# Kernel tuning notes

Measured on AMD Instinct MI355X. Metric: run time of the kernel, lower is better.

## Reference

```python
import jax, jax.numpy as jnp
import numpy as np

B, S, HID = 1, 2048, 2048
H = 16
D_NOPE, D_ROPE, D_V = 128, 64, 128
Q_HEAD = D_NOPE + D_ROPE  # 192
QL, KVL = 1536, 512
EPS = 1e-6
SCALE = Q_HEAD ** -0.5


def rms_norm(x, w, eps=EPS):
    return x * jax.lax.rsqrt(jnp.mean(x * x, axis=-1, keepdims=True) + eps) * w


def rotate_half(x):
    h = x.shape[-1] // 2
    return jnp.concatenate([-x[..., h:], x[..., :h]], axis=-1)


def apply_rope(x, cos, sin):
    # DeepSeek de-interleave: view(..., d//2, 2).transpose(-1,-2).reshape == [even, odd]
    x = jnp.concatenate([x[..., 0::2], x[..., 1::2]], axis=-1)
    return x * cos + rotate_half(x) * sin


def setup_inputs() -> dict:
    key = jax.random.key(0)
    ks = jax.random.split(key, 8)
    x = jax.random.normal(ks[0], (B, S, HID), dtype=jnp.float32)
    # causal additive mask
    causal = jnp.tril(jnp.ones((S, S), dtype=bool))
    mask = jnp.where(causal, 0.0, -1e9).astype(jnp.float32)[None, None]
    position_ids = jnp.broadcast_to(jnp.arange(S, dtype=jnp.int32), (B, S))
    # RoPE caches, theta=10000
    inv_freq = 1.0 / (10000.0 ** (np.arange(0, D_ROPE, 2, dtype=np.float32) / D_ROPE))
    freqs = np.outer(np.arange(S, dtype=np.float32), inv_freq)
    emb = np.concatenate([freqs, freqs], axis=-1)
    cos = jnp.asarray(np.cos(emb), dtype=jnp.float32)
    sin = jnp.asarray(np.sin(emb), dtype=jnp.float32)
    w = lambda k, shp: (jax.random.normal(k, shp, dtype=jnp.float32) * 0.02)
    return {
        "x": x, "mask": mask, "position_ids": position_ids, "cos": cos, "sin": sin,
        "q_a_w": w(ks[1], (HID, QL)),
        "q_a_ln": jnp.ones((QL,), jnp.float32),
        "q_b_w": w(ks[2], (QL, H * Q_HEAD)),
        "kv_a_w": w(ks[3], (HID, KVL + D_ROPE)),
        "kv_a_ln": jnp.ones((KVL,), jnp.float32),
        "kv_b_w": w(ks[4], (KVL, H * (D_NOPE + D_V))),
        "o_w": w(ks[5], (H * D_V, HID)),
    }


def reference(x, mask, position_ids, cos, sin, q_a_w, q_a_ln, q_b_w, kv_a_w, kv_a_ln, kv_b_w, o_w):
    b, s, _ = x.shape
    # low-rank Q projection
    q = rms_norm(x @ q_a_w, q_a_ln) @ q_b_w            # [B,S,H*192]
    q = q.reshape(b, s, H, Q_HEAD).transpose(0, 2, 1, 3)  # [B,H,S,192]
    q_nope, q_pe = q[..., :D_NOPE], q[..., D_NOPE:]
    # compressed KV + decoupled rope key (MQA, shared across heads)
    ckv = x @ kv_a_w                                   # [B,S,512+64]
    c_norm = rms_norm(ckv[..., :KVL], kv_a_ln)         # [B,S,512]
    k_pe = ckv[..., KVL:][:, None]                     # [B,1,S,64]
    kv = (c_norm @ kv_b_w).reshape(b, s, H, D_NOPE + D_V).transpose(0, 2, 1, 3)
    k_nope, value = kv[..., :D_NOPE], kv[..., D_NOPE:]  # [B,H,S,128] each
    # rope
    cos_p = cos[position_ids][:, None]                 # [B,1,S,64]
    sin_p = sin[position_ids][:, None]
    q_pe = apply_rope(q_pe, cos_p, sin_p)
    k_pe = apply_rope(k_pe, cos_p, sin_p)
    query = jnp.concatenate([q_nope, q_pe], axis=-1)   # [B,H,S,192]
    key = jnp.concatenate([k_nope, jnp.broadcast_to(k_pe, (b, H, s, D_ROPE))], axis=-1)
    scores = jnp.einsum("bhsd,bhtd->bhst", query, key) * SCALE + mask
    attn = jax.nn.softmax(scores, axis=-1)
    out = jnp.einsum("bhst,bhtd->bhsd", attn, value)   # [B,H,S,128]
    out = out.transpose(0, 2, 1, 3).reshape(b, s, H * D_V) @ o_w
    kv_cache = jnp.concatenate([c_norm, k_pe[:, 0]], axis=-1)  # [B,S,576] latent cache
    return out, kv_cache
```

## Files before the change

### kernel.cpp

```cpp
#include <hip/hip_runtime.h>

typedef unsigned short u16;
typedef __bf16 bf16x8 __attribute__((ext_vector_type(8)));
typedef short s16x4 __attribute__((ext_vector_type(4)));
typedef short s16x8 __attribute__((ext_vector_type(8)));
typedef float f32x4 __attribute__((ext_vector_type(4)));

#define S_LEN 2048
#define NHEAD 16
#define QHEAD 192
#define EPS 1e-6f
#define ATTN_SCALE 0.07216878364870323f
#define QSCALE_LOG2E 0.10412011228586118f

__device__ __forceinline__ u16 f2bf(float f) {
    unsigned u = __builtin_bit_cast(unsigned, f);
    u = (u + 0x7FFFu + ((u >> 16) & 1u)) >> 16;
    return (u16)u;
}
__device__ __forceinline__ float bf2f(u16 h) {
    unsigned u = ((unsigned)h) << 16;
    return __builtin_bit_cast(float, u);
}

__device__ __forceinline__ void gl_lds16(const u16* g, u16* l) {
    __builtin_amdgcn_global_load_lds(
        (const __attribute__((address_space(1))) unsigned int*)g,
        (__attribute__((address_space(3))) unsigned int*)l,
        16, 0, 0);
}

#if defined(__has_builtin) && __has_builtin(__builtin_amdgcn_mfma_f32_16x16x16bf16_1k)
__device__ __forceinline__ f32x4 mfma16(s16x4 a, s16x4 b, f32x4 c) {
    return __builtin_amdgcn_mfma_f32_16x16x16bf16_1k(a, b, c, 0, 0, 0);
}
#else
__device__ __forceinline__ f32x4 mfma16(s16x4 a, s16x4 b, f32x4 c) {
    asm volatile("v_mfma_f32_16x16x16_bf16 %0, %1, %2, %0"
                 : "+v"(c) : "v"(a), "v"(b));
    return c;
}
#endif

template <int CF32>
__device__ __forceinline__ void gemm_core(
    u16* __restrict__ smem,
    const u16* __restrict__ A, const u16* __restrict__ B, void* __restrict__ Cv,
    int K, int lda, int ldb, int ldc, int tm, int tn)
{
    const int tid = threadIdx.x;
    const int w = tid >> 6, lane = tid & 63;
    const int q = lane >> 4, r = lane & 15;

    const int lr = lane & 15;
    const int lc = (lane >> 4) * 8;
    const u16* ga0 = A + (long)(tm * 128 + w * 32 + lr) * lda + lc;
    const u16* ga1 = ga0 + 16 * (long)lda;
    const u16* gb0 = B + (long)(tn * 128 + w * 32 + lr) * ldb + lc;
    const u16* gb1 = gb0 + 16 * (long)ldb;
    const int sa0 = w * 1024, sa1 = sa0 + 512;
    const int sb0 = 4096 + w * 1024, sb1 = sb0 + 512;

    f32x4 acc[4][4] = {};
    const int wm = w >> 1;
    const int wn = w & 1;
    const int n = K >> 6;

    gl_lds16(ga0, smem + sa0);
    gl_lds16(ga1, smem + sa1);
    gl_lds16(gb0, smem + sb0);
    gl_lds16(gb1, smem + sb1);
    gl_lds16(ga0 + 32, smem + 8192 + sa0);
    gl_lds16(ga1 + 32, smem + 8192 + sa1);
    gl_lds16(gb0 + 32, smem + 8192 + sb0);
    gl_lds16(gb1 + 32, smem + 8192 + sb1);
    asm volatile("s_waitcnt vmcnt(0)" ::: "memory");
    __builtin_amdgcn_sched_barrier(0);
    __builtin_amdgcn_s_barrier();
    __builtin_amdgcn_sched_barrier(0);

    for (int t = 0; t < n; ++t) {
        u16* const cur = smem + (t & 1) * 16384;
        u16* const nxt = smem + ((t + 1) & 1) * 16384;
        if (t + 1 < n) {
            const long k1 = (long)(t + 1) << 6;
            gl_lds16(ga0 + k1, nxt + sa0);
            gl_lds16(ga1 + k1, nxt + sa1);
            gl_lds16(gb0 + k1, nxt + sb0);
            gl_lds16(gb1 + k1, nxt + sb1);
            gl_lds16(ga0 + k1 + 32, nxt + 8192 + sa0);
            gl_lds16(ga1 + k1 + 32, nxt + 8192 + sa1);
            gl_lds16(gb0 + k1 + 32, nxt + 8192 + sb0);
            gl_lds16(gb1 + k1 + 32, nxt + 8192 + sb1);
        }
        #pragma unroll
        for (int kk = 0; kk < 2; ++kk) {
            u16* const sub = cur + kk * 8192;
            bf16x8 af[4], bv[4];
            #pragma unroll
            for (int mt = 0; mt < 4; ++mt)
                af[mt] = *(const bf16x8*)&sub[(wm * 4 + mt) * 512 + lane * 8];
            #pragma unroll
            for (int nt = 0; nt < 4; ++nt)
                bv[nt] = *(const bf16x8*)&sub[4096 + (wn * 4 + nt) * 512 + lane * 8];
            #pragma unroll
            for (int mt = 0; mt < 4; ++mt)
                #pragma unroll
                for (int nt = 0; nt < 4; ++nt)
                    acc[mt][nt] = __builtin_amdgcn_mfma_f32_16x16x32_bf16(
                        af[mt], bv[nt], acc[mt][nt], 0, 0, 0);
        }
        if (t + 1 < n) {
            asm volatile("s_waitcnt vmcnt(0)" ::: "memory");
            __builtin_amdgcn_sched_barrier(0);
            __builtin_amdgcn_s_barrier();
            __builtin_amdgcn_sched_barrier(0);
        }
    }

    const int row0 = tm * 128 + wm * 64 + q * 4;
    const int col0 = tn * 128 + wn * 64 + r;
    if (CF32) {
        float* C = (float*)Cv;
        #pragma unroll
        for (int mt = 0; mt < 4; ++mt)
            #pragma unroll
            for (int i = 0; i < 4; ++i) {
                long rb = (long)(row0 + mt * 16 + i) * ldc + col0;
                #pragma unroll
                for (int nt = 0; nt < 4; ++nt)
                    C[rb + nt * 16] = acc[mt][nt][i];
            }
    } else {
        u16* C = (u16*)Cv;
        #pragma unroll
        for (int mt = 0; mt < 4; ++mt)
            #pragma unroll
            for (int i = 0; i < 4; ++i) {
                long rb = (long)(row0 + mt * 16 + i) * ldc + col0;
                #pragma unroll
                for (int nt = 0; nt < 4; ++nt)
                    C[rb + nt * 16] = f2bf(acc[mt][nt][i]);
            }
    }
}

__global__ __launch_bounds__(256, 2)
void gemm_ks(const u16* __restrict__ A, const u16* __restrict__ B,
             float* __restrict__ C0, float* __restrict__ C1,
             int Kh, int lda, int ldb, int ldc)
{
    __shared__ __align__(16) u16 smem[2 * 16384];
    const int z = blockIdx.z;
    float* C = z ? C1 : C0;
    gemm_core<1>(smem, A + (long)z * Kh, B + (long)z * Kh, C,
                 Kh, lda, ldb, ldc, blockIdx.y, blockIdx.x);
}

__global__ __launch_bounds__(256, 2)
void gemm_bt_dual(const u16* __restrict__ A0, const u16* __restrict__ B0,
                  void* __restrict__ C0, int K0, int lda0, int ldb0, int ldc0, int nx0,
                  const u16* __restrict__ A1, const u16* __restrict__ B1,
                  void* __restrict__ C1, int K1, int lda1, int ldb1, int ldc1, int nx1)
{
    __shared__ __align__(16) u16 smem[2 * 16384];
    if (blockIdx.z == 0) {
        if ((int)blockIdx.x >= nx0) return;
        gemm_core<0>(smem, A0, B0, C0, K0, lda0, ldb0, ldc0,
                     blockIdx.y, blockIdx.x);
    } else {
        if ((int)blockIdx.x >= nx1) return;
        gemm_core<0>(smem, A1, B1, C1, K1, lda1, ldb1, ldc1,
                     blockIdx.y, blockIdx.x);
    }
}

__global__ __launch_bounds__(256)
void addout_k(float4* __restrict__ out, const float4* __restrict__ p)
{
    int i = blockIdx.x * 256 + threadIdx.x;
    float4 a = out[i], b = p[i];
    a.x += b.x; a.y += b.y; a.z += b.z; a.w += b.w;
    out[i] = a;
}

template<int C0, int C1>
__device__ __forceinline__ void stage_tile(
    const u16* __restrict__ kvb, const u16* __restrict__ kpe,
    const u16* __restrict__ vt,
    u16* __restrict__ Kl, u16* __restrict__ Vl,
    int h, int t, int quad, int r)
{
    #pragma unroll
    for (int c = C0; c < C1; ++c) {
        if (c < 24) {
            const int mtk = c / 6, kc = c % 6;
            const int row = t * 64 + mtk * 16 + r;
            const u16* src = (kc < 4)
                ? kvb + (size_t)row * 4096 + h * 256 + kc * 32 + quad * 8
                : kpe + (size_t)row * 64 + (kc - 4) * 32 + quad * 8;
            gl_lds16(src, &Kl[c * 512]);
        } else {
            const int cv = c - 24, mtd = cv >> 1, sc = cv & 1;
            const u16* src = vt + ((size_t)h * 128 + mtd * 16 + r) * 2048
                             + t * 64 + sc * 32 + quad * 8;
            gl_lds16(src, &Vl[cv * 512]);
        }
    }
}

__device__ __forceinline__ void stage_dispatch(
    const u16* __restrict__ kvb, const u16* __restrict__ kpe,
    const u16* __restrict__ vt,
    u16* __restrict__ Kl, u16* __restrict__ Vl,
    int w, int h, int t, int quad, int r)
{
    if (w == 0)      stage_tile<0, 10>(kvb, kpe, vt, Kl, Vl, h, t, quad, r);
    else if (w == 1) stage_tile<10, 20>(kvb, kpe, vt, Kl, Vl, h, t, quad, r);
    else if (w == 2) stage_tile<20, 30>(kvb, kpe, vt, Kl, Vl, h, t, quad, r);
    else             stage_tile<30, 40>(kvb, kpe, vt, Kl, Vl, h, t, quad, r);
}

__device__ __forceinline__ void kv_tile_step(
    const u16* __restrict__ Kl, const u16* __restrict__ Vl,
    const bf16x8 (&Qf)[6], f32x4 (&Oacc)[8], float& lsum,
    int lane, int quad, int r, int kglob0, int qg, bool maskT)
{
    f32x4 Sacc[4];
    #pragma unroll
    for (int mtk = 0; mtk < 4; ++mtk)
        Sacc[mtk] = (f32x4){0.f, 0.f, 0.f, 0.f};
    #pragma unroll
    for (int kc = 0; kc < 6; ++kc)
        #pragma unroll
        for (int mtk = 0; mtk < 4; ++mtk) {
            bf16x8 Ak = *(const bf16x8*)&Kl[(mtk * 6 + kc) * 512 + lane * 8];
            Sacc[mtk] = __builtin_amdgcn_mfma_f32_16x16x32_bf16(
                Ak, Qf[kc], Sacc[mtk], 0, 0, 0);
        }
    #pragma unroll
    for (int sc = 0; sc < 2; ++sc) {
        s16x4 Pf[2];
        #pragma unroll
        for (int half = 0; half < 2; ++half) {
            const int kb = sc * 2 + half;
            const int kb0 = kglob0 + kb * 16 + quad * 4;
            #pragma unroll
            for (int i = 0; i < 4; ++i) {
                float pv = exp2f(Sacc[kb][i]);
                if (maskT && (kb0 + i > qg)) pv = 0.f;
                lsum += pv;
                Pf[half][i] = (short)f2bf(pv);
            }
        }
        #pragma unroll
        for (int mtd = 0; mtd < 8; ++mtd) {
            s16x8 Av8 = *(const s16x8*)&Vl[(mtd * 2 + sc) * 512 + quad * 128 + r * 8];
            s16x4 lo = __builtin_shufflevector(Av8, Av8, 0, 1, 2, 3);
            s16x4 hi = __builtin_shufflevector(Av8, Av8, 4, 5, 6, 7);
            Oacc[mtd] = mfma16(lo, Pf[0], Oacc[mtd]);
            Oacc[mtd] = mfma16(hi, Pf[1], Oacc[mtd]);
        }
    }
}

__global__ __launch_bounds__(256, 2)
void flash_attn(const u16* __restrict__ query, const u16* __restrict__ kvb,
                const u16* __restrict__ kpe, const u16* __restrict__ vt,
                u16* __restrict__ ao)
{
    const int tid = threadIdx.x;
    const int w = tid >> 6, lane = tid & 63;
    const int quad = lane >> 4, r = lane & 15;

    const int bid = (int)blockIdx.x;
    const int i = bid & 255;
    const int t_ = i >> 4;
    const int h = i & 15;
    const int j = (bid < 256) ? (31 - t_) : t_;

    const int q0 = j * 64;
    const int ntk = j + 1;

    __shared__ __align__(16) u16 smem[40960];

    const int qg = q0 + w * 16 + r;

    bf16x8 Qf[6];
    #pragma unroll
    for (int kc = 0; kc < 6; ++kc)
        Qf[kc] = *(const bf16x8*)(query
            + ((size_t)h * S_LEN + q0 + w * 16 + r) * QHEAD
            + kc * 32 + quad * 8);

    f32x4 Oacc[8];
    #pragma unroll
    for (int mtd = 0; mtd < 8; ++mtd)
        Oacc[mtd] = (f32x4){0.f, 0.f, 0.f, 0.f};
    float lsum = 0.f;

    stage_dispatch(kvb, kpe, vt, smem, smem + 12288, w, h, 0, quad, r);
    __syncthreads();

    for (int t = 0; t < ntk; ++t) {
        u16* const curb = smem + (t & 1) * 20480;
        u16* const nxtb = smem + ((t + 1) & 1) * 20480;
        if (t + 1 < ntk)
            stage_dispatch(kvb, kpe, vt, nxtb, nxtb + 12288, w, h, t + 1, quad, r);
        kv_tile_step(curb, curb + 12288, Qf, Oacc, lsum,
                     lane, quad, r, t * 64, qg, t == ntk - 1);
        __syncthreads();
    }

    float l = lsum;
    l += __shfl_xor(l, 16, 64);
    l += __shfl_xor(l, 32, 64);
    const float inv = 1.0f / l;
    const int qrow = q0 + w * 16 + r;
    #pragma unroll
    for (int mtd = 0; mtd < 8; ++mtd) {
        ushort4 o;
        o.x = f2bf(Oacc[mtd][0] * inv);
        o.y = f2bf(Oacc[mtd][1] * inv);
        o.z = f2bf(Oacc[mtd][2] * inv);
        o.w = f2bf(Oacc[mtd][3] * inv);
        *(ushort4*)(ao + (size_t)qrow * 2048 + h * 128 + mtd * 16 + quad * 4) = o;
    }
}

__device__ __forceinline__ void wtrans_body(
    float (*tile)[33], const float* __restrict__ in, u16* __restrict__ out,
    int K, int N, int bx, int by, int tid)
{
    const int tx = tid & 31, ty = tid >> 5;
    const int k0 = bx * 32, n0 = by * 32;
    #pragma unroll
    for (int jj = 0; jj < 32; jj += 8) {
        int nn = n0 + tx;
        tile[ty + jj][tx] = (nn < N) ? in[(long)(k0 + ty + jj) * N + nn] : 0.0f;
    }
    __syncthreads();
    #pragma unroll
    for (int jj = 0; jj < 32; jj += 8)
        out[(long)(n0 + ty + jj) * K + k0 + tx] = f2bf(tile[tx][ty + jj]);
}

__global__ __launch_bounds__(256)
void prep_k(const float4* __restrict__ x4, ushort4* __restrict__ xb4,
            const float* __restrict__ q_a_w, const float* __restrict__ kv_a_w,
            const float* __restrict__ q_b_w, const float* __restrict__ kv_b_w,
            const float* __restrict__ o_w,
            u16* __restrict__ W1, u16* __restrict__ qbwt,
            u16* __restrict__ kvbwt, u16* __restrict__ owt)
{
    __shared__ float tile[32][33];
    const int tid = threadIdx.x;
    int b = (int)blockIdx.x;
    if (b < 4096) {
        int i = b * 256 + tid;
        float4 v = x4[i];
        ushort4 o;
        o.x = f2bf(v.x); o.y = f2bf(v.y); o.z = f2bf(v.z); o.w = f2bf(v.w);
        xb4[i] = o;
        return;
    }
    b -= 4096;
    if (b < 3072)       wtrans_body(tile, q_a_w,  W1,                  2048, 1536, b % 64, b / 64, tid);
    else if ((b -= 3072) < 1280) wtrans_body(tile, kv_a_w, W1 + 1536ULL * 2048, 2048, 576,  b % 64, b / 64, tid);
    else if ((b -= 1280) < 4608) wtrans_body(tile, q_b_w,  qbwt,       1536, 3072, b % 48, b / 48, tid);
    else if ((b -= 4608) < 2048) wtrans_body(tile, kv_b_w, kvbwt,      512,  4096, b % 16, b / 16, tid);
    else { b -= 2048;            wtrans_body(tile, o_w,    owt,        2048, 2048, b % 64, b / 64, tid); }
}

__global__ __launch_bounds__(256)
void norm_k(const float* __restrict__ pa, const float* __restrict__ pb,
            u16* __restrict__ qkv, const float* __restrict__ q_ln,
            const float* __restrict__ kv_ln, const int* __restrict__ pos_ids,
            const float* __restrict__ cosb, const float* __restrict__ sinb,
            float* __restrict__ kvout, u16* __restrict__ cnb,
            u16* __restrict__ kpe)
{
    const int s = blockIdx.x, tid = threadIdx.x;
    __shared__ float rowbuf[2176];
    __shared__ float red[8];
    const long base = (long)s * 2176;
    float sum1 = 0.f, sum2 = 0.f;
    for (int d = tid; d < 2176; d += 256) {
        float v = pa[base + d] + pb[base + d];
        rowbuf[d] = v;
        if (d < 1536)      sum1 += v * v;
        else if (d < 2048) sum2 += v * v;
    }
    #pragma unroll
    for (int o = 32; o; o >>= 1) {
        sum1 += __shfl_xor(sum1, o, 64);
        sum2 += __shfl_xor(sum2, o, 64);
    }
    if ((tid & 63) == 0) { red[tid >> 6] = sum1; red[4 + (tid >> 6)] = sum2; }
    __syncthreads();
    sum1 = red[0] + red[1] + red[2] + red[3];
    sum2 = red[4] + red[5] + red[6] + red[7];
    const float sc1 = rsqrtf(sum1 / 1536.f + EPS);
    const float sc2 = rsqrtf(sum2 / 512.f + EPS);
    for (int d = tid; d < 1536; d += 256)
        qkv[base + d] = f2bf(rowbuf[d] * sc1 * q_ln[d]);
    for (int d = tid; d < 512; d += 256) {
        float v = rowbuf[1536 + d] * sc2 * kv_ln[d];
        kvout[(long)s * 576 + d] = v;
        cnb[(long)s * 512 + d] = f2bf(v);
    }
    if (tid < 32) {
        int p = pos_ids[s];
        float x0 = rowbuf[2048 + 2 * tid];
        float x1 = rowbuf[2048 + 2 * tid + 1];
        float c1 = cosb[p * 64 + tid], s1 = sinb[p * 64 + tid];
        float c2 = cosb[p * 64 + 32 + tid], s2 = sinb[p * 64 + 32 + tid];
        float lo = x0 * c1 - x1 * s1;
        float hi = x1 * c2 + x0 * s2;
        kvout[(long)s * 576 + 512 + tid] = lo;
        kvout[(long)s * 576 + 544 + tid] = hi;
        kpe[(long)s * 64 + tid] = f2bf(lo);
        kpe[(long)s * 64 + 32 + tid] = f2bf(hi);
    }
}

__global__ __launch_bounds__(256)
void post_k(const u16* __restrict__ qb, const int* __restrict__ pos_ids,
            const float* __restrict__ cosb, const float* __restrict__ sinb,
            u16* __restrict__ query, const u16* __restrict__ kv,
            u16* __restrict__ vt)
{
    __shared__ u16 tile[32][33];
    const int tid = threadIdx.x;
    int b = (int)blockIdx.x;
    if (b < 2048) {
        const int s = b;
        const u16* row = qb + (long)s * 3072;
        {
            int h = tid >> 4, c = tid & 15;
            const u16* src = &row[h * QHEAD + c * 8];
            u16* dst = &query[((long)(h * S_LEN + s)) * QHEAD + c * 8];
            ushort4 a = *(const ushort4*)src;
            ushort4 bb = *(const ushort4*)(src + 4);
            ushort4 oa, ob;
            oa.x = f2bf(bf2f(a.x) * QSCALE_LOG2E); oa.y = f2bf(bf2f(a.y) * QSCALE_LOG2E);
            oa.z = f2bf(bf2f(a.z) * QSCALE_LOG2E); oa.w = f2bf(bf2f(a.w) * QSCALE_LOG2E);
            ob.x = f2bf(bf2f(bb.x) * QSCALE_LOG2E); ob.y = f2bf(bf2f(bb.y) * QSCALE_LOG2E);
            ob.z = f2bf(bf2f(bb.z) * QSCALE_LOG2E); ob.w = f2bf(bf2f(bb.w) * QSCALE_LOG2E);
            *(ushort4*)dst = oa;
            *(ushort4*)(dst + 4) = ob;
        }
        int p = pos_ids[s];
        for (int idx = tid; idx < 512; idx += 256) {
            int h = idx >> 5, i = idx & 31;
            float x0 = bf2f(row[h * QHEAD + 128 + 2 * i]);
            float x1 = bf2f(row[h * QHEAD + 128 + 2 * i + 1]);
            float c1 = cosb[p * 64 + i], s1 = sinb[p * 64 + i];
            float c2 = cosb[p * 64 + 32 + i], s2 = sinb[p * 64 + 32 + i];
            u16* qr = query + ((long)(h * S_LEN + s)) * QHEAD;
            qr[128 + i] = f2bf((x0 * c1 - x1 * s1) * QSCALE_LOG2E);
            qr[160 + i] = f2bf((x1 * c2 + x0 * s2) * QSCALE_LOG2E);
        }
    } else {
        b -= 2048;
        const int s0 = (b & 63) * 32, d0 = ((b >> 6) & 3) * 32, h = b >> 8;
        const int tx = tid & 31, ty = tid >> 5;
        #pragma unroll
        for (int jj = 0; jj < 32; jj += 8)
            tile[ty + jj][tx] = kv[(long)(s0 + ty + jj) * 4096 + h * 256 + 128 + d0 + tx];
        __syncthreads();
        const int txp = ((tx >> 2) & 3) * 8 + (tx >> 4) * 4 + (tx & 3);
        #pragma unroll
        for (int jj = 0; jj < 32; jj += 8)
            vt[(long)(h * 128 + d0 + ty + jj) * S_LEN + s0 + txp] = tile[tx][ty + jj];
    }
}

extern "C" void kernel_launch(void* const* d_in, const int* in_sizes, int n_in,
                              void* d_out, int out_size, void* d_ws, size_t ws_size,
                              hipStream_t stream)
{
    const float* x      = (const float*)d_in[0];
    const int*   posid  = (const int*)d_in[2];
    const float* cosb   = (const float*)d_in[3];
    const float* sinb   = (const float*)d_in[4];
    const float* q_a_w  = (const float*)d_in[5];
    const float* q_a_ln = (const float*)d_in[6];
    const float* q_b_w  = (const float*)d_in[7];
    const float* kv_a_w = (const float*)d_in[8];
    const float* kv_a_ln= (const float*)d_in[9];
    const float* kv_b_w = (const float*)d_in[10];
    const float* o_w    = (const float*)d_in[11];

    float* out    = (float*)d_out;
    float* kv_out = out + (size_t)2048 * 2048;

    char* ws = (char*)d_ws;
    size_t off = 0;
    auto alloc = [&](size_t bytes) { char* p = ws + off; off += (bytes + 255) & ~(size_t)255; return p; };
    u16* xb    = (u16*)alloc(2048ULL * 2048 * 2);
    u16* W1    = (u16*)alloc(2176ULL * 2048 * 2);
    u16* qbwt  = (u16*)alloc(3072ULL * 1536 * 2);
    u16* kvbwt = (u16*)alloc(4096ULL * 512 * 2);
    u16* owt   = (u16*)alloc(2048ULL * 2048 * 2);
    u16* qkv_a = (u16*)alloc(2048ULL * 2176 * 2);
    u16* qbuf  = (u16*)alloc(2048ULL * 3072 * 2);
    u16* query = (u16*)alloc(16ULL * 2048 * 192 * 2);
    u16* cnb   = (u16*)alloc(2048ULL * 512 * 2);
    u16* kpe   = (u16*)alloc(2048ULL * 64 * 2);
    u16* kvbuf = (u16*)alloc(2048ULL * 4096 * 2);
    u16* vt    = (u16*)alloc(16ULL * 128 * 2048 * 2);
    u16* ao    = (u16*)alloc(2048ULL * 2048 * 2);
    (void)ws_size; (void)in_sizes; (void)n_in; (void)out_size;

    float* g1p0 = (float*)qbuf;
    float* g1p1 = (float*)kvbuf;
    float* g5p  = (float*)xb;

    dim3 blk(256);

    prep_k<<<dim3(19200), blk, 0, stream>>>(
        (const float4*)x, (ushort4*)xb, q_a_w, kv_a_w, q_b_w, kv_b_w, o_w,
        W1, qbwt, kvbwt, owt);

    gemm_ks<<<dim3(17, 16, 2), blk, 0, stream>>>(
        xb, W1, g1p0, g1p1, 1024, 2048, 2048, 2176);

    norm_k<<<dim3(2048), blk, 0, stream>>>(g1p0, g1p1, qkv_a, q_a_ln, kv_a_ln,
                                           posid, cosb, sinb, kv_out, cnb, kpe);

    gemm_bt_dual<<<dim3(32, 16, 2), blk, 0, stream>>>(
        qkv_a, qbwt, qbuf, 1536, 2176, 1536, 3072, 24,
        cnb, kvbwt, kvbuf, 512, 512, 512, 4096, 32);

    post_k<<<dim3(6144), blk, 0, stream>>>(qbuf, posid, cosb, sinb, query, kvbuf, vt);

    flash_attn<<<dim3(512), dim3(256), 0, stream>>>(query, kvbuf, kpe, vt, ao);

    gemm_ks<<<dim3(16, 16, 2), blk, 0, stream>>>(
        ao, owt, g5p, out, 1024, 2048, 2048, 2048);
    addout_k<<<dim3(4096), blk, 0, stream>>>((float4*)out, (const float4*)g5p);
}
```

Measured before the change: 390.6 us.

## Split attention KV range across two blocks, merge partials, overlap weight transposes with GEMM

Flash attention now splits each query tile's KV loop into two halves handled by separate blocks (1024 blocks instead of 512). Each block writes unnormalized fp32 partial outputs and row sums, and a new merge kernel combines them into bf16. The q_b, kv_b and o weight transposes move out of the prep kernel and into the first GEMM's launch as extra blocks, so that work overlaps with the GEMM. s_setprio is raised around the attention compute step. The split adds fp32 partial traffic and an extra launch, and depends on workspace aliasing (PA on xb, PB on qbwt, lp on cnb) being safe at that point in the pipeline.

```diff
diff --git a/kernel.cpp b/kernel.cpp
--- a/kernel.cpp
+++ b/kernel.cpp
@@ -145,6 +145,23 @@
     }
 }
 
+__device__ __forceinline__ void wtrans_body(
+    float (*tile)[33], const float* __restrict__ in, u16* __restrict__ out,
+    int K, int N, int bx, int by, int tid)
+{
+    const int tx = tid & 31, ty = tid >> 5;
+    const int k0 = bx * 32, n0 = by * 32;
+    #pragma unroll
+    for (int jj = 0; jj < 32; jj += 8) {
+        int nn = n0 + tx;
+        tile[ty + jj][tx] = (nn < N) ? in[(long)(k0 + ty + jj) * N + nn] : 0.0f;
+    }
+    __syncthreads();
+    #pragma unroll
+    for (int jj = 0; jj < 32; jj += 8)
+        out[(long)(n0 + ty + jj) * K + k0 + tx] = f2bf(tile[tx][ty + jj]);
+}
+
 __global__ __launch_bounds__(256, 2)
 void gemm_ks(const u16* __restrict__ A, const u16* __restrict__ B,
              float* __restrict__ C0, float* __restrict__ C1,
@@ -155,6 +172,30 @@
     float* C = z ? C1 : C0;
     gemm_core<1>(smem, A + (long)z * Kh, B + (long)z * Kh, C,
                  Kh, lda, ldb, ldc, blockIdx.y, blockIdx.x);
+}
+
+__global__ __launch_bounds__(256, 2)
+void gemm1p(const u16* __restrict__ xb, const u16* __restrict__ W1,
+            float* __restrict__ C0, float* __restrict__ C1,
+            const float* __restrict__ q_b_w, const float* __restrict__ kv_b_w,
+            const float* __restrict__ o_w,
+            u16* __restrict__ qbwt, u16* __restrict__ kvbwt, u16* __restrict__ owt)
+{
+    __shared__ __align__(16) u16 smem[2 * 16384];
+    const int tid = threadIdx.x;
+    int b = (int)blockIdx.x;
+    if (b < 544) {
+        const int z = b >= 272;
+        const int bb = b - z * 272;
+        gemm_core<1>(smem, xb + (long)z * 1024, W1 + (long)z * 1024,
+                     z ? C1 : C0, 1024, 2048, 2048, 2176, bb / 17, bb % 17);
+        return;
+    }
+    b -= 544;
+    float (*tile)[33] = (float(*)[33])smem;
+    if (b < 4608)                wtrans_body(tile, q_b_w,  qbwt,  1536, 3072, b % 48, b / 48, tid);
+    else if ((b -= 4608) < 2048) wtrans_body(tile, kv_b_w, kvbwt, 512,  4096, b % 16, b / 16, tid);
+    else { b -= 2048;            wtrans_body(tile, o_w,    owt,   2048, 2048, b % 64, b / 64, tid); }
 }
 
 __global__ __launch_bounds__(256, 2)
@@ -226,6 +267,7 @@
     const bf16x8 (&Qf)[6], f32x4 (&Oacc)[8], float& lsum,
     int lane, int quad, int r, int kglob0, int qg, bool maskT)
 {
+    __builtin_amdgcn_s_setprio(1);
     f32x4 Sacc[4];
     #pragma unroll
     for (int mtk = 0; mtk < 4; ++mtk)
@@ -262,25 +304,32 @@
             Oacc[mtd] = mfma16(hi, Pf[1], Oacc[mtd]);
         }
     }
+    __builtin_amdgcn_s_setprio(0);
 }
 
 __global__ __launch_bounds__(256, 2)
 void flash_attn(const u16* __restrict__ query, const u16* __restrict__ kvb,
                 const u16* __restrict__ kpe, const u16* __restrict__ vt,
-                u16* __restrict__ ao)
+                float* __restrict__ PA, float* __restrict__ PB,
+                float* __restrict__ lp)
 {
     const int tid = threadIdx.x;
     const int w = tid >> 6, lane = tid & 63;
     const int quad = lane >> 4, r = lane & 15;
 
     const int bid = (int)blockIdx.x;
-    const int i = bid & 255;
+    const int hf = bid >> 9;
+    const int p = bid & 511;
+    const int i = p & 255;
     const int t_ = i >> 4;
     const int h = i & 15;
-    const int j = (bid < 256) ? (31 - t_) : t_;
+    const int j = (p < 256) ? (31 - t_) : t_;
 
     const int q0 = j * 64;
-    const int ntk = j + 1;
+    const int nfull = j + 1;
+    const int sp = (nfull + 1) >> 1;
+    const int t0 = hf ? sp : 0;
+    const int t1 = hf ? nfull : sp;
 
     __shared__ __align__(16) u16 smem[40960];
 
@@ -299,59 +348,66 @@
         Oacc[mtd] = (f32x4){0.f, 0.f, 0.f, 0.f};
     float lsum = 0.f;
 
-    stage_dispatch(kvb, kpe, vt, smem, smem + 12288, w, h, 0, quad, r);
+    if (t0 < t1)
+        stage_dispatch(kvb, kpe, vt, smem, smem + 12288, w, h, t0, quad, r);
     __syncthreads();
 
-    for (int t = 0; t < ntk; ++t) {
-        u16* const curb = smem + (t & 1) * 20480;
-        u16* const nxtb = smem + ((t + 1) & 1) * 20480;
-        if (t + 1 < ntk)
+    for (int t = t0; t < t1; ++t) {
+        u16* const curb = smem + ((t - t0) & 1) * 20480;
+        u16* const nxtb = smem + ((t - t0 + 1) & 1) * 20480;
+        if (t + 1 < t1)
             stage_dispatch(kvb, kpe, vt, nxtb, nxtb + 12288, w, h, t + 1, quad, r);
         kv_tile_step(curb, curb + 12288, Qf, Oacc, lsum,
-                     lane, quad, r, t * 64, qg, t == ntk - 1);
+                     lane, quad, r, t * 64, qg, t == nfull - 1);
         __syncthreads();
     }
 
     float l = lsum;
     l += __shfl_xor(l, 16, 64);
     l += __shfl_xor(l, 32, 64);
-    const float inv = 1.0f / l;
-    const int qrow = q0 + w * 16 + r;
-    #pragma unroll
-    for (int mtd = 0; mtd < 8; ++mtd) {
+    float* OP = hf ? PB : PA;
+    const long pb = ((long)p * 64 + w * 16 + r) * 128;
+    #pragma unroll
+    for (int mtd = 0; mtd < 8; ++mtd)
+        *(f32x4*)&OP[pb + mtd * 16 + quad * 4] = Oacc[mtd];
+    if (quad == 0)
+        lp[hf * 32768 + p * 64 + w * 16 + r] = l;
+}
+
+__global__ __launch_bounds__(256)
+void merge_k(const float* __restrict__ PA, const float* __restrict__ PB,
+             const float* __restrict__ lp, u16* __restrict__ ao)
+{
+    const int p = (int)blockIdx.x, tid = threadIdx.x;
+    const int i = p & 255;
+    const int t_ = i >> 4;
+    const int h = i & 15;
+    const int j = (p < 256) ? (31 - t_) : t_;
+    const int q0 = j * 64;
+    const int row = tid >> 2;
+    const int cseg = (tid & 3) * 32;
+    const float lA = lp[p * 64 + row];
+    const float lB = lp[32768 + p * 64 + row];
+    const float inv = 1.0f / (lA + lB);
+    const long base = ((long)p * 64 + row) * 128 + cseg;
+    u16* dst = ao + (size_t)(q0 + row) * 2048 + h * 128 + cseg;
+    #pragma unroll
+    for (int k = 0; k < 8; ++k) {
+        f32x4 va = *(const f32x4*)&PA[base + k * 4];
+        f32x4 vb = *(const f32x4*)&PB[base + k * 4];
         ushort4 o;
-        o.x = f2bf(Oacc[mtd][0] * inv);
-        o.y = f2bf(Oacc[mtd][1] * inv);
-        o.z = f2bf(Oacc[mtd][2] * inv);
-        o.w = f2bf(Oacc[mtd][3] * inv);
-        *(ushort4*)(ao + (size_t)qrow * 2048 + h * 128 + mtd * 16 + quad * 4) = o;
-    }
-}
-
-__device__ __forceinline__ void wtrans_body(
-    float (*tile)[33], const float* __restrict__ in, u16* __restrict__ out,
-    int K, int N, int bx, int by, int tid)
-{
-    const int tx = tid & 31, ty = tid >> 5;
-    const int k0 = bx * 32, n0 = by * 32;
-    #pragma unroll
-    for (int jj = 0; jj < 32; jj += 8) {
-        int nn = n0 + tx;
-        tile[ty + jj][tx] = (nn < N) ? in[(long)(k0 + ty + jj) * N + nn] : 0.0f;
-    }
-    __syncthreads();
-    #pragma unroll
-    for (int jj = 0; jj < 32; jj += 8)
-        out[(long)(n0 + ty + jj) * K + k0 + tx] = f2bf(tile[tx][ty + jj]);
+        o.x = f2bf((va[0] + vb[0]) * inv);
+        o.y = f2bf((va[1] + vb[1]) * inv);
+        o.z = f2bf((va[2] + vb[2]) * inv);
+        o.w = f2bf((va[3] + vb[3]) * inv);
+        *(ushort4*)(dst + k * 4) = o;
+    }
 }
 
 __global__ __launch_bounds__(256)
 void prep_k(const float4* __restrict__ x4, ushort4* __restrict__ xb4,
             const float* __restrict__ q_a_w, const float* __restrict__ kv_a_w,
-            const float* __restrict__ q_b_w, const float* __restrict__ kv_b_w,
-            const float* __restrict__ o_w,
-            u16* __restrict__ W1, u16* __restrict__ qbwt,
-            u16* __restrict__ kvbwt, u16* __restrict__ owt)
+            u16* __restrict__ W1)
 {
     __shared__ float tile[32][33];
     const int tid = threadIdx.x;
@@ -365,11 +421,8 @@
         return;
     }
     b -= 4096;
-    if (b < 3072)       wtrans_body(tile, q_a_w,  W1,                  2048, 1536, b % 64, b / 64, tid);
-    else if ((b -= 3072) < 1280) wtrans_body(tile, kv_a_w, W1 + 1536ULL * 2048, 2048, 576,  b % 64, b / 64, tid);
-    else if ((b -= 1280) < 4608) wtrans_body(tile, q_b_w,  qbwt,       1536, 3072, b % 48, b / 48, tid);
-    else if ((b -= 4608) < 2048) wtrans_body(tile, kv_b_w, kvbwt,      512,  4096, b % 16, b / 16, tid);
-    else { b -= 2048;            wtrans_body(tile, o_w,    owt,        2048, 2048, b % 64, b / 64, tid); }
+    if (b < 3072) wtrans_body(tile, q_a_w, W1, 2048, 1536, b % 64, b / 64, tid);
+    else { b -= 3072; wtrans_body(tile, kv_a_w, W1 + 1536ULL * 2048, 2048, 576, b % 64, b / 64, tid); }
 }
 
 __global__ __launch_bounds__(256)
@@ -500,9 +553,9 @@
     auto alloc = [&](size_t bytes) { char* p = ws + off; off += (bytes + 255) & ~(size_t)255; return p; };
     u16* xb    = (u16*)alloc(2048ULL * 2048 * 2);
     u16* W1    = (u16*)alloc(2176ULL * 2048 * 2);
+    u16* owt   = (u16*)alloc(2048ULL * 2048 * 2);
     u16* qbwt  = (u16*)alloc(3072ULL * 1536 * 2);
     u16* kvbwt = (u16*)alloc(4096ULL * 512 * 2);
-    u16* owt   = (u16*)alloc(2048ULL * 2048 * 2);
     u16* qkv_a = (u16*)alloc(2048ULL * 2176 * 2);
     u16* qbuf  = (u16*)alloc(2048ULL * 3072 * 2);
     u16* query = (u16*)alloc(16ULL * 2048 * 192 * 2);
@@ -515,16 +568,18 @@
 
     float* g1p0 = (float*)qbuf;
     float* g1p1 = (float*)kvbuf;
+    float* PA   = (float*)xb;
+    float* PB   = (float*)qbwt;
+    float* lp   = (float*)cnb;
     float* g5p  = (float*)xb;
 
     dim3 blk(256);
 
-    prep_k<<<dim3(19200), blk, 0, stream>>>(
-        (const float4*)x, (ushort4*)xb, q_a_w, kv_a_w, q_b_w, kv_b_w, o_w,
-        W1, qbwt, kvbwt, owt);
-
-    gemm_ks<<<dim3(17, 16, 2), blk, 0, stream>>>(
-        xb, W1, g1p0, g1p1, 1024, 2048, 2048, 2176);
+    prep_k<<<dim3(8448), blk, 0, stream>>>(
+        (const float4*)x, (ushort4*)xb, q_a_w, kv_a_w, W1);
+
+    gemm1p<<<dim3(11296), blk, 0, stream>>>(
+        xb, W1, g1p0, g1p1, q_b_w, kv_b_w, o_w, qbwt, kvbwt, owt);
 
     norm_k<<<dim3(2048), blk, 0, stream>>>(g1p0, g1p1, qkv_a, q_a_ln, kv_a_ln,
                                            posid, cosb, sinb, kv_out, cnb, kpe);
@@ -535,7 +590,9 @@
 
     post_k<<<dim3(6144), blk, 0, stream>>>(qbuf, posid, cosb, sinb, query, kvbuf, vt);
 
-    flash_attn<<<dim3(512), dim3(256), 0, stream>>>(query, kvbuf, kpe, vt, ao);
+    flash_attn<<<dim3(1024), blk, 0, stream>>>(query, kvbuf, kpe, vt, PA, PB, lp);
+
+    merge_k<<<dim3(512), blk, 0, stream>>>(PA, PB, lp, ao);
 
     gemm_ks<<<dim3(16, 16, 2), blk, 0, stream>>>(
         ao, owt, g5p, out, 1024, 2048, 2048, 2048);
```

Result: slower. 406.9 us (+4.2%).
